# Kernel tuning notes

Hardware: AMD Instinct MI355X
Metric: run time of the kernel (lower is better)

## Reference

```python
import jax, jax.numpy as jnp
import numpy as np

INPUT_SIZE = 2048
H1 = 256
H2 = 64
NB = 8
BATCH = 16384


def setup_inputs() -> dict:
    key = jax.random.key(0)
    ks = jax.random.split(key, 8)
    x = jax.random.normal(ks[0], (BATCH, INPUT_SIZE), dtype=jnp.float32)
    bucket_indices = jax.random.randint(ks[1], (BATCH,), 0, NB, dtype=jnp.int32)
    # torch nn.Linear weights: (out_features, in_features), bias: (out_features,)
    def lin(k, fan_in, fan_out):
        kw, kb = jax.random.split(k)
        bound = 1.0 / np.sqrt(fan_in)
        W = jax.random.uniform(kw, (fan_out, fan_in), jnp.float32, -bound, bound)
        b = jax.random.uniform(kb, (fan_out,), jnp.float32, -bound, bound)
        return W, b
    W1, b1 = lin(ks[2], INPUT_SIZE, H1 * NB)
    W2, b2 = lin(ks[3], H1, H2 * NB)
    W3, b3 = lin(ks[4], H2, 1 * NB)
    return {"x": x, "bucket_indices": bucket_indices,
            "W1": W1, "b1": b1, "W2": W2, "b2": b2, "W3": W3, "b3": b3}


def _gather_bucket(all_out, idx, width):
    # all_out: (B, NB*width) -> select per-sample bucket slice -> (B, width)
    B = all_out.shape[0]
    per = all_out.reshape(B, NB, width)
    return jnp.take_along_axis(per, idx[:, None, None], axis=1)[:, 0, :]


def reference(x, bucket_indices, W1, b1, W2, b2, W3, b3):
    idx = bucket_indices.astype(jnp.int32)
    h1_all = x @ W1.T + b1                      # (B, H1*NB)
    h1 = jnp.clip(_gather_bucket(h1_all, idx, H1), 0.0, 1.0)
    h2_all = h1 @ W2.T + b2                     # (B, H2*NB)
    h2 = jnp.clip(_gather_bucket(h2_all, idx, H2), 0.0, 1.0)
    out_all = h2 @ W3.T + b3                    # (B, NB)
    out = _gather_bucket(out_all, idx, 1)       # (B, 1)
    return out[:, :, None]                      # (B, 1, 1) matches unsqueeze(-1)
```

## Files before the change

### kernel.cpp

```cpp
#include <hip/hip_runtime.h>

#define INSZ   2048
#define NH1    256
#define NH2    64
#define NB     8
#define BATCH  16384

#define TS        32
#define MAXTILES  (BATCH / TS)
#define GRIDX     (NB * MAXTILES)

#define W1F_U4   (NB * 64 * 16 * 64)
#define W2F_U4   (NB * 8 * 4 * 64)

#define META_OFF  0
#define ORDER_OFF 1024
#define W1F_OFF   (1024 + BATCH * 4)
#define W2F_OFF   (W1F_OFF + W1F_U4 * 16)
#define WS_NEED   (W2F_OFF + W2F_U4 * 16)

typedef float f2  __attribute__((ext_vector_type(2)));
typedef float f4  __attribute__((ext_vector_type(4)));
typedef float f32x4 __attribute__((ext_vector_type(4)));
typedef short bf16x8 __attribute__((ext_vector_type(8)));

__device__ __forceinline__ unsigned short f2bf(float f) {
    unsigned u = __float_as_uint(f);
    u += 0x7fffu + ((u >> 16) & 1u);
    return (unsigned short)(u >> 16);
}
__device__ __forceinline__ float clamp01(float v) { return fminf(fmaxf(v, 0.0f), 1.0f); }
__device__ __forceinline__ unsigned pack2(float a, float b) {
    return (unsigned)f2bf(a) | ((unsigned)f2bf(b) << 16);
}


__global__ void k_countscan(const int* __restrict__ idx, int* __restrict__ meta) {
    __shared__ int scnt[NB];
    int t = threadIdx.x;
    if (t < NB) scnt[t] = 0;
    __syncthreads();
    int local[NB];
#pragma unroll
    for (int bb = 0; bb < NB; bb++) local[bb] = 0;
    for (int i = t; i < BATCH; i += 1024) {
        int b = idx[i];
#pragma unroll
        for (int bb = 0; bb < NB; bb++) local[bb] += (b == bb) ? 1 : 0;
    }
#pragma unroll
    for (int bb = 0; bb < NB; bb++) {
        int v = local[bb];
        v += __shfl_xor(v, 1);  v += __shfl_xor(v, 2);  v += __shfl_xor(v, 4);
        v += __shfl_xor(v, 8);  v += __shfl_xor(v, 16); v += __shfl_xor(v, 32);
        if ((t & 63) == 0) atomicAdd(&scnt[bb], v);
    }
    __syncthreads();
    if (t == 0) {
        int run = 0;
        for (int b = 0; b < NB; b++) {
            int c = scnt[b];
            meta[b]      = c;
            meta[8 + b]  = run;
            meta[16 + b] = run;
            run += c;
        }
    }
}

__global__ void k_scatter(const int* __restrict__ idx, int* __restrict__ meta,
                          int* __restrict__ order) {
    __shared__ int wcnt[16][NB];
    __shared__ int sbase[NB];
    int t = threadIdx.x;
    int i = blockIdx.x * 1024 + t;
    int b = idx[i];
    int wv = t >> 6, lane = t & 63;
    unsigned long long mymask = 0;
#pragma unroll
    for (int bb = 0; bb < NB; bb++) {
        unsigned long long m = __ballot(b == bb);
        if (b == bb) mymask = m;
        if (lane == bb) wcnt[wv][bb] = (int)__popcll(m);
    }
    int myrank = (int)__popcll(mymask & ((1ull << lane) - 1ull));
    __syncthreads();
    if (t < NB) {
        int sum = 0;
        for (int w2 = 0; w2 < 16; w2++) { int c = wcnt[w2][t]; wcnt[w2][t] = sum; sum += c; }
        sbase[t] = atomicAdd(&meta[16 + t], sum);
    }
    __syncthreads();
    order[sbase[b] + wcnt[wv][b] + myrank] = i;
}

__global__ void k_pack(const float* __restrict__ W1, const float* __restrict__ W2,
                       uint4* __restrict__ W1f, uint4* __restrict__ W2f) {
    int u = blockIdx.x * 256 + threadIdx.x;
    if (u < W1F_U4) {
        int lane = u & 63, cb = (u >> 6) & 15, kb = (u >> 10) & 63, bkt = u >> 16;
        int l15 = lane & 15, quad = lane >> 4;
        const float* p = W1 + (size_t)(bkt * NH1 + cb * 16 + l15) * INSZ + kb * 32 + quad * 8;
        f4 lo = *(const f4*)p, hi = *(const f4*)(p + 4);
        uint4 o;
        o.x = pack2(lo[0], lo[1]); o.y = pack2(lo[2], lo[3]);
        o.z = pack2(hi[0], hi[1]); o.w = pack2(hi[2], hi[3]);
        W1f[u] = o;
    } else {
        int v = u - W1F_U4;
        if (v >= W2F_U4) return;
        int lane = v & 63, cg2 = (v >> 6) & 3, kb2 = (v >> 8) & 7, bkt = v >> 11;
        int l15 = lane & 15, quad = lane >> 4;
        const float* p = W2 + (size_t)(bkt * NH2 + cg2 * 16 + l15) * NH1 + kb2 * 32 + quad * 8;
        f4 lo = *(const f4*)p, hi = *(const f4*)(p + 4);
        uint4 o;
        o.x = pack2(lo[0], lo[1]); o.y = pack2(lo[2], lo[3]);
        o.z = pack2(hi[0], hi[1]); o.w = pack2(hi[2], hi[3]);
        W2f[v] = o;
    }
}


__global__ __launch_bounds__(512, 4) void fused_v10(
    const float* __restrict__ x, const int* __restrict__ meta,
    const int* __restrict__ order,
    const short* __restrict__ W1f, const short* __restrict__ W2f,
    const float* __restrict__ b1, const float* __restrict__ b2,
    const float* __restrict__ W3, const float* __restrict__ b3,
    float* __restrict__ out)
{
    const int bkt  = blockIdx.x & 7;
    const int tile = blockIdx.x >> 3;
    const int cnt  = meta[bkt];
    const int base = tile * TS;
    if (base >= cnt) return;
    const int off = meta[8 + bkt];

    __shared__ short sX[2][TS * 40];
    __shared__ short sh1[TS * 264];
    __shared__ float sPart[4][TS];

    const int t = threadIdx.x;
    const int lane = t & 63, w = t >> 6;
    const int l15 = lane & 15, quad = lane >> 4;

    const int xr = t >> 4, kq = t & 15;
    int ir = base + xr; if (ir > cnt - 1) ir = cnt - 1;
    const float* xtp = x + (size_t)order[off + ir] * INSZ + kq * 2;
    const int sxo = xr * 40 + kq * 2;

    const short* wp = W1f + ((size_t)bkt << 19) + (size_t)(2 * w) * 512 + lane * 8;

    f32x4 acc[2][2];
#pragma unroll
    for (int f = 0; f < 2; f++)
#pragma unroll
        for (int j = 0; j < 2; j++) acc[f][j] = (f32x4)0.0f;

    bf16x8 wA0, wA1, wB0, wB1;
    f2 xs0, xs1, xs2, xs3;

    wA0 = *(const bf16x8*)(wp);
    wA1 = *(const bf16x8*)(wp + 512);
    wB0 = *(const bf16x8*)(wp + 8192);
    wB1 = *(const bf16x8*)(wp + 8192 + 512);
    {
        f2 x0 = *(const f2*)xtp;
        xs1 = *(const f2*)(xtp + 32);
        xs2 = *(const f2*)(xtp + 64);
        xs3 = *(const f2*)(xtp + 96);
        *(unsigned*)&sX[0][sxo] = pack2(x0[0], x0[1]);
    }

#define L1_STEP(KB, XL, XW, WU0, WU1)                                                   \
    {                                                                                   \
        if ((KB) < 60) XL = *(const f2*)(xtp + ((KB) + 4) * 32);                        \
        asm volatile("s_waitcnt lgkmcnt(0)" ::: "memory");                              \
        __builtin_amdgcn_s_barrier();                                                   \
        asm volatile("" ::: "memory");                                                  \
        const int P = (KB) & 1;                                                         \
        bf16x8 a0 = *(const bf16x8*)&sX[P][(l15)      * 40 + quad * 8];                 \
        bf16x8 a1 = *(const bf16x8*)&sX[P][(16 + l15) * 40 + quad * 8];                 \
        acc[0][0] = __builtin_amdgcn_mfma_f32_16x16x32_bf16(a0, WU0, acc[0][0], 0,0,0); \
        acc[0][1] = __builtin_amdgcn_mfma_f32_16x16x32_bf16(a0, WU1, acc[0][1], 0,0,0); \
        acc[1][0] = __builtin_amdgcn_mfma_f32_16x16x32_bf16(a1, WU0, acc[1][0], 0,0,0); \
        acc[1][1] = __builtin_amdgcn_mfma_f32_16x16x32_bf16(a1, WU1, acc[1][1], 0,0,0); \
        if ((KB) < 63) {                                                                \
            *(unsigned*)&sX[P ^ 1][sxo] = pack2(XW[0], XW[1]);                          \
        }                                                                               \
        if ((KB) < 62) {                                                                \
            WU0 = *(const bf16x8*)(wp + (size_t)((KB) + 2) * 8192);                     \
            WU1 = *(const bf16x8*)(wp + (size_t)((KB) + 2) * 8192 + 512);               \
        }                                                                               \
    }

#pragma unroll 1
    for (int kb = 0; kb < 64; kb += 4) {
        L1_STEP(kb + 0, xs0, xs1, wA0, wA1)
        L1_STEP(kb + 1, xs1, xs2, wB0, wB1)
        L1_STEP(kb + 2, xs2, xs3, wA0, wA1)
        L1_STEP(kb + 3, xs3, xs0, wB0, wB1)
    }
#undef L1_STEP

#pragma unroll
    for (int j = 0; j < 2; j++) {
        int col = w * 32 + j * 16 + l15;
        float bias = b1[bkt * NH1 + col];
#pragma unroll
        for (int f = 0; f < 2; f++)
#pragma unroll
            for (int r = 0; r < 4; r++) {
                int row = f * 16 + quad * 4 + r;
                sh1[row * 264 + col] = (short)f2bf(clamp01(acc[f][j][r] + bias));
            }
    }
    __syncthreads();

    const int rw = w & 1, cg2 = w >> 1;
    f32x4 c2 = (f32x4)0.0f;
    const short* w2p = W2f + (size_t)bkt * 16384 + lane * 8;
#pragma unroll
    for (int kb2 = 0; kb2 < 8; kb2++) {
        bf16x8 a2 = *(const bf16x8*)&sh1[(rw * 16 + l15) * 264 + kb2 * 32 + quad * 8];
        bf16x8 bw = *(const bf16x8*)(w2p + (kb2 * 4 + cg2) * 512);
        c2 = __builtin_amdgcn_mfma_f32_16x16x32_bf16(a2, bw, c2, 0, 0, 0);
    }

    {
        int n2 = cg2 * 16 + l15;
        float bias2 = b2[bkt * NH2 + n2];
        float w3v   = W3[bkt * NH2 + n2];
        float s[4];
#pragma unroll
        for (int r = 0; r < 4; r++)
            s[r] = clamp01(c2[r] + bias2) * w3v;
#pragma unroll
        for (int r = 0; r < 4; r++) {
            float pp = s[r];
            pp += __shfl_xor(pp, 1); pp += __shfl_xor(pp, 2);
            pp += __shfl_xor(pp, 4); pp += __shfl_xor(pp, 8);
            if (l15 == 0) sPart[cg2][rw * 16 + quad * 4 + r] = pp;
        }
    }
    __syncthreads();
    if (t < TS && base + t < cnt)
        out[order[off + base + t]] =
            sPart[0][t] + sPart[1][t] + sPart[2][t] + sPart[3][t] + b3[bkt];
}


__global__ void naive_mlp(const float* __restrict__ x, const int* __restrict__ idx,
                          const float* __restrict__ W1, const float* __restrict__ b1,
                          const float* __restrict__ W2, const float* __restrict__ b2,
                          const float* __restrict__ W3, const float* __restrict__ b3,
                          float* __restrict__ out)
{
    int i = blockIdx.x;
    int b = idx[i];
    __shared__ float sx[INSZ];
    __shared__ float sh1n[NH1];
    __shared__ float sh2n[NH2];
    for (int t = threadIdx.x; t < INSZ; t += 256) sx[t] = x[(size_t)i * INSZ + t];
    __syncthreads();
    int j = threadIdx.x;
    {
        const float* wr = W1 + (size_t)(b * NH1 + j) * INSZ;
        float acc = b1[b * NH1 + j];
        for (int k = 0; k < INSZ; k++) acc += sx[k] * wr[k];
        sh1n[j] = fminf(fmaxf(acc, 0.f), 1.f);
    }
    __syncthreads();
    if (j < NH2) {
        const float* wr = W2 + (size_t)(b * NH2 + j) * NH1;
        float acc = b2[b * NH2 + j];
        for (int k = 0; k < NH1; k++) acc += sh1n[k] * wr[k];
        sh2n[j] = fminf(fmaxf(acc, 0.f), 1.f);
    }
    __syncthreads();
    if (j == 0) {
        float acc = b3[b];
        for (int k = 0; k < NH2; k++) acc += sh2n[k] * W3[b * NH2 + k];
        out[i] = acc;
    }
}

extern "C" void kernel_launch(void* const* d_in, const int* in_sizes, int n_in,
                              void* d_out, int out_size, void* d_ws, size_t ws_size,
                              hipStream_t stream) {
    const float* x  = (const float*)d_in[0];
    const int* bidx = (const int*)d_in[1];
    const float* W1 = (const float*)d_in[2];
    const float* b1 = (const float*)d_in[3];
    const float* W2 = (const float*)d_in[4];
    const float* b2 = (const float*)d_in[5];
    const float* W3 = (const float*)d_in[6];
    const float* b3 = (const float*)d_in[7];
    float* out = (float*)d_out;

    if (ws_size >= (size_t)WS_NEED) {
        char* ws = (char*)d_ws;
        int*   meta  = (int*)(ws + META_OFF);
        int*   order = (int*)(ws + ORDER_OFF);
        uint4* W1f   = (uint4*)(ws + W1F_OFF);
        uint4* W2f   = (uint4*)(ws + W2F_OFF);

        k_countscan<<<1, 1024, 0, stream>>>(bidx, meta);
        k_scatter<<<BATCH / 1024, 1024, 0, stream>>>(bidx, meta, order);
        k_pack<<<(W1F_U4 + W2F_U4) / 256, 256, 0, stream>>>(W1, W2, W1f, W2f);
        fused_v10<<<GRIDX, 512, 0, stream>>>(x, meta, order,
                                             (const short*)W1f, (const short*)W2f,
                                             b1, b2, W3, b3, out);
    } else {
        naive_mlp<<<BATCH, 256, 0, stream>>>(x, bidx, W1, b1, W2, b2, W3, b3, out);
    }
}
```

Before: 276.6 us.

## Stage x in large 512-wide LDS chunks and coalesce weight-pack reads

The layer-1 loop no longer double-buffers x at 32-column granularity with a barrier every k-step. It now loads 512 columns of x per stage as float4 reads into a 16-slab padded LDS buffer and runs 16 MFMA k-steps per barrier, cutting the number of barriers. The pack kernel now reads W1/W2 rows contiguously and scatters its output into the MFMA fragment layout, so the source reads are coalesced. In exchange LDS grows to about 37 KB and launch bounds drop to 2 blocks per CU. Weight loads are no longer register-prefetched two steps ahead, so latency hiding now relies on unrolling.

```diff
diff --git a/kernel.cpp b/kernel.cpp
--- a/kernel.cpp
+++ b/kernel.cpp
@@ -19,7 +19,6 @@
 #define W2F_OFF   (W1F_OFF + W1F_U4 * 16)
 #define WS_NEED   (W2F_OFF + W2F_U4 * 16)
 
-typedef float f2  __attribute__((ext_vector_type(2)));
 typedef float f4  __attribute__((ext_vector_type(4)));
 typedef float f32x4 __attribute__((ext_vector_type(4)));
 typedef short bf16x8 __attribute__((ext_vector_type(8)));
@@ -32,6 +31,11 @@
 __device__ __forceinline__ float clamp01(float v) { return fminf(fmaxf(v, 0.0f), 1.0f); }
 __device__ __forceinline__ unsigned pack2(float a, float b) {
     return (unsigned)f2bf(a) | ((unsigned)f2bf(b) << 16);
+}
+__device__ __forceinline__ bf16x8 mk8(uint2 lo, uint2 hi) {
+    union { unsigned u[4]; bf16x8 v; } r;
+    r.u[0] = lo.x; r.u[1] = lo.y; r.u[2] = hi.x; r.u[3] = hi.y;
+    return r.v;
 }
 
 
@@ -98,30 +102,34 @@
                        uint4* __restrict__ W1f, uint4* __restrict__ W2f) {
     int u = blockIdx.x * 256 + threadIdx.x;
     if (u < W1F_U4) {
-        int lane = u & 63, cb = (u >> 6) & 15, kb = (u >> 10) & 63, bkt = u >> 16;
-        int l15 = lane & 15, quad = lane >> 4;
-        const float* p = W1 + (size_t)(bkt * NH1 + cb * 16 + l15) * INSZ + kb * 32 + quad * 8;
+        int k8 = u & 255, row = (u >> 8) & 255, bkt = u >> 16;
+        int kb = k8 >> 2, quad = k8 & 3;
+        int cb = row >> 4, l15 = row & 15;
+        const float* p = W1 + ((size_t)(bkt * NH1 + row)) * INSZ + k8 * 8;
         f4 lo = *(const f4*)p, hi = *(const f4*)(p + 4);
         uint4 o;
         o.x = pack2(lo[0], lo[1]); o.y = pack2(lo[2], lo[3]);
         o.z = pack2(hi[0], hi[1]); o.w = pack2(hi[2], hi[3]);
-        W1f[u] = o;
+        W1f[((bkt * 64 + kb) * 16 + cb) * 64 + quad * 16 + l15] = o;
     } else {
         int v = u - W1F_U4;
         if (v >= W2F_U4) return;
-        int lane = v & 63, cg2 = (v >> 6) & 3, kb2 = (v >> 8) & 7, bkt = v >> 11;
-        int l15 = lane & 15, quad = lane >> 4;
-        const float* p = W2 + (size_t)(bkt * NH2 + cg2 * 16 + l15) * NH1 + kb2 * 32 + quad * 8;
+        int k8 = v & 31, row = (v >> 5) & 63, bkt = v >> 11;
+        int kb2 = k8 >> 2, quad = k8 & 3;
+        int cg2 = row >> 4, l15 = row & 15;
+        const float* p = W2 + ((size_t)(bkt * NH2 + row)) * NH1 + k8 * 8;
         f4 lo = *(const f4*)p, hi = *(const f4*)(p + 4);
         uint4 o;
         o.x = pack2(lo[0], lo[1]); o.y = pack2(lo[2], lo[3]);
         o.z = pack2(hi[0], hi[1]); o.w = pack2(hi[2], hi[3]);
-        W2f[v] = o;
-    }
-}
-
-
-__global__ __launch_bounds__(512, 4) void fused_v10(
+        W2f[((bkt * 8 + kb2) * 4 + cg2) * 64 + quad * 16 + l15] = o;
+    }
+}
+
+
+#define MFMA16 __builtin_amdgcn_mfma_f32_16x16x32_bf16
+
+__global__ __launch_bounds__(512, 2) void fused_v13(
     const float* __restrict__ x, const int* __restrict__ meta,
     const int* __restrict__ order,
     const short* __restrict__ W1f, const short* __restrict__ W2f,
@@ -136,7 +144,7 @@
     if (base >= cnt) return;
     const int off = meta[8 + bkt];
 
-    __shared__ short sX[2][TS * 40];
+    __shared__ short sX[16 * 1152];
     __shared__ short sh1[TS * 264];
     __shared__ float sPart[4][TS];
 
@@ -144,10 +152,9 @@
     const int lane = t & 63, w = t >> 6;
     const int l15 = lane & 15, quad = lane >> 4;
 
-    const int xr = t >> 4, kq = t & 15;
+    const int xr = t >> 4, c16 = t & 15;
     int ir = base + xr; if (ir > cnt - 1) ir = cnt - 1;
-    const float* xtp = x + (size_t)order[off + ir] * INSZ + kq * 2;
-    const int sxo = xr * 40 + kq * 2;
+    const float* xrow = x + (size_t)order[off + ir] * INSZ;
 
     const short* wp = W1f + ((size_t)bkt << 19) + (size_t)(2 * w) * 512 + lane * 8;
 
@@ -157,51 +164,37 @@
 #pragma unroll
         for (int j = 0; j < 2; j++) acc[f][j] = (f32x4)0.0f;
 
-    bf16x8 wA0, wA1, wB0, wB1;
-    f2 xs0, xs1, xs2, xs3;
-
-    wA0 = *(const bf16x8*)(wp);
-    wA1 = *(const bf16x8*)(wp + 512);
-    wB0 = *(const bf16x8*)(wp + 8192);
-    wB1 = *(const bf16x8*)(wp + 8192 + 512);
-    {
-        f2 x0 = *(const f2*)xtp;
-        xs1 = *(const f2*)(xtp + 32);
-        xs2 = *(const f2*)(xtp + 64);
-        xs3 = *(const f2*)(xtp + 96);
-        *(unsigned*)&sX[0][sxo] = pack2(x0[0], x0[1]);
-    }
-
-#define L1_STEP(KB, XL, XW, WU0, WU1)                                                   \
-    {                                                                                   \
-        if ((KB) < 60) XL = *(const f2*)(xtp + ((KB) + 4) * 32);                        \
-        asm volatile("s_waitcnt lgkmcnt(0)" ::: "memory");                              \
-        __builtin_amdgcn_s_barrier();                                                   \
-        asm volatile("" ::: "memory");                                                  \
-        const int P = (KB) & 1;                                                         \
-        bf16x8 a0 = *(const bf16x8*)&sX[P][(l15)      * 40 + quad * 8];                 \
-        bf16x8 a1 = *(const bf16x8*)&sX[P][(16 + l15) * 40 + quad * 8];                 \
-        acc[0][0] = __builtin_amdgcn_mfma_f32_16x16x32_bf16(a0, WU0, acc[0][0], 0,0,0); \
-        acc[0][1] = __builtin_amdgcn_mfma_f32_16x16x32_bf16(a0, WU1, acc[0][1], 0,0,0); \
-        acc[1][0] = __builtin_amdgcn_mfma_f32_16x16x32_bf16(a1, WU0, acc[1][0], 0,0,0); \
-        acc[1][1] = __builtin_amdgcn_mfma_f32_16x16x32_bf16(a1, WU1, acc[1][1], 0,0,0); \
-        if ((KB) < 63) {                                                                \
-            *(unsigned*)&sX[P ^ 1][sxo] = pack2(XW[0], XW[1]);                          \
-        }                                                                               \
-        if ((KB) < 62) {                                                                \
-            WU0 = *(const bf16x8*)(wp + (size_t)((KB) + 2) * 8192);                     \
-            WU1 = *(const bf16x8*)(wp + (size_t)((KB) + 2) * 8192 + 512);               \
-        }                                                                               \
-    }
-
 #pragma unroll 1
-    for (int kb = 0; kb < 64; kb += 4) {
-        L1_STEP(kb + 0, xs0, xs1, wA0, wA1)
-        L1_STEP(kb + 1, xs1, xs2, wB0, wB1)
-        L1_STEP(kb + 2, xs2, xs3, wA0, wA1)
-        L1_STEP(kb + 3, xs3, xs0, wB0, wB1)
-    }
-#undef L1_STEP
+    for (int s = 0; s < 4; s++) {
+        if (s) __syncthreads();
+#pragma unroll
+        for (int j = 0; j < 8; j++) {
+            const int col = s * 512 + c16 * 4 + j * 64;
+            f4 v = *(const f4*)(xrow + col);
+            const int kbL = (col >> 5) & 15, ko = col & 31;
+            uint2 pk; pk.x = pack2(v[0], v[1]); pk.y = pack2(v[2], v[3]);
+            *(uint2*)&sX[kbL * 1152 + xr * 36 + ko] = pk;
+        }
+        __syncthreads();
+
+#pragma unroll
+        for (int kbL = 0; kbL < 16; kbL++) {
+            const int kb = s * 16 + kbL;
+            const int ab = kbL * 1152 + l15 * 36 + quad * 8;
+            uint2 lo0 = *(const uint2*)&sX[ab];
+            uint2 hi0 = *(const uint2*)&sX[ab + 4];
+            uint2 lo1 = *(const uint2*)&sX[ab + 576];
+            uint2 hi1 = *(const uint2*)&sX[ab + 580];
+            bf16x8 a0 = mk8(lo0, hi0);
+            bf16x8 a1 = mk8(lo1, hi1);
+            bf16x8 w0 = *(const bf16x8*)(wp + (size_t)kb * 8192);
+            bf16x8 w1 = *(const bf16x8*)(wp + (size_t)kb * 8192 + 512);
+            acc[0][0] = MFMA16(a0, w0, acc[0][0], 0, 0, 0);
+            acc[0][1] = MFMA16(a0, w1, acc[0][1], 0, 0, 0);
+            acc[1][0] = MFMA16(a1, w0, acc[1][0], 0, 0, 0);
+            acc[1][1] = MFMA16(a1, w1, acc[1][1], 0, 0, 0);
+        }
+    }
 
 #pragma unroll
     for (int j = 0; j < 2; j++) {
@@ -224,20 +217,20 @@
     for (int kb2 = 0; kb2 < 8; kb2++) {
         bf16x8 a2 = *(const bf16x8*)&sh1[(rw * 16 + l15) * 264 + kb2 * 32 + quad * 8];
         bf16x8 bw = *(const bf16x8*)(w2p + (kb2 * 4 + cg2) * 512);
-        c2 = __builtin_amdgcn_mfma_f32_16x16x32_bf16(a2, bw, c2, 0, 0, 0);
+        c2 = MFMA16(a2, bw, c2, 0, 0, 0);
     }
 
     {
         int n2 = cg2 * 16 + l15;
         float bias2 = b2[bkt * NH2 + n2];
         float w3v   = W3[bkt * NH2 + n2];
-        float s[4];
+        float sacc[4];
 #pragma unroll
         for (int r = 0; r < 4; r++)
-            s[r] = clamp01(c2[r] + bias2) * w3v;
+            sacc[r] = clamp01(c2[r] + bias2) * w3v;
 #pragma unroll
         for (int r = 0; r < 4; r++) {
-            float pp = s[r];
+            float pp = sacc[r];
             pp += __shfl_xor(pp, 1); pp += __shfl_xor(pp, 2);
             pp += __shfl_xor(pp, 4); pp += __shfl_xor(pp, 8);
             if (l15 == 0) sPart[cg2][rw * 16 + quad * 4 + r] = pp;
@@ -308,7 +301,7 @@
         k_countscan<<<1, 1024, 0, stream>>>(bidx, meta);
         k_scatter<<<BATCH / 1024, 1024, 0, stream>>>(bidx, meta, order);
         k_pack<<<(W1F_U4 + W2F_U4) / 256, 256, 0, stream>>>(W1, W2, W1f, W2f);
-        fused_v10<<<GRIDX, 512, 0, stream>>>(x, meta, order,
+        fused_v13<<<GRIDX, 512, 0, stream>>>(x, meta, order,
                                              (const short*)W1f, (const short*)W2f,
                                              b1, b2, W3, b3, out);
     } else {
```

Result: no change. 275.3 us (-0.5%).
